# Optimization experiments

Hardware: AMD Instinct MI355X
Metric: run time of the kernel (lower is better)

## Reference

```python
import jax, jax.numpy as jnp
import numpy as np

GAMMA = 0.5
POLY_COEF = 0.1
POLY_DEGREE = 3


def setup_inputs() -> dict:
    key = jax.random.key(0)
    kx, ky = jax.random.split(key)
    x = jax.random.normal(kx, (8192, 256), dtype=jnp.float32)
    y = jax.random.normal(ky, (8192, 256), dtype=jnp.float32)
    return {"x": x, "y": y}


def reference(x, y):
    # K(x, y) = exp(-gamma * ||x - y||^2) + poly_coef * (x.y^T + 1)^degree
    xy = x @ y.T                                   # (N, M) GEMM
    x2 = jnp.sum(x * x, axis=-1, keepdims=True)    # (N, 1)
    y2 = jnp.sum(y * y, axis=-1)[None, :]          # (1, M)
    sqdist = jnp.maximum(x2 + y2 - 2.0 * xy, 0.0)
    rbf = jnp.exp(-GAMMA * sqdist)
    poly = POLY_COEF * (xy + 1.0) ** POLY_DEGREE
    return rbf + poly
```

## Files before the change

### kernel.cpp

```cpp
#include <hip/hip_runtime.h>
#include <hip/hip_bf16.h>
#include <cstdint>
#include <cstddef>


#define NROWS 8192
#define DK    256
#define BM    128
#define BN    128
#define BK    64

typedef __bf16 bf16_8 __attribute__((ext_vector_type(8)));
typedef float  f32x4  __attribute__((ext_vector_type(4)));

__device__ __forceinline__ unsigned short f2bf(float f) {
    unsigned int u = __builtin_bit_cast(unsigned int, f);
    u = (u + 0x7FFFu + ((u >> 16) & 1u)) >> 16;
    return (unsigned short)u;
}

__global__ __launch_bounds__(64) void prep_kernel(
    const float* __restrict__ x, const float* __restrict__ y,
    unsigned short* __restrict__ xb, unsigned short* __restrict__ yb,
    float* __restrict__ x2, float* __restrict__ y2)
{
    const int row  = blockIdx.x;
    const int lane = threadIdx.x;
    const size_t base = (size_t)row * DK + lane * 4;

    const float4 vx = *(const float4*)(x + base);
    const float4 vy = *(const float4*)(y + base);

    ushort4 hx = make_ushort4(f2bf(vx.x), f2bf(vx.y), f2bf(vx.z), f2bf(vx.w));
    ushort4 hy = make_ushort4(f2bf(vy.x), f2bf(vy.y), f2bf(vy.z), f2bf(vy.w));
    *(ushort4*)(xb + base) = hx;
    *(ushort4*)(yb + base) = hy;

    float sx = vx.x * vx.x + vx.y * vx.y + vx.z * vx.z + vx.w * vx.w;
    float sy = vy.x * vy.x + vy.y * vy.y + vy.z * vy.z + vy.w * vy.w;
    #pragma unroll
    for (int off = 32; off > 0; off >>= 1) {
        sx += __shfl_down(sx, off);
        sy += __shfl_down(sy, off);
    }
    if (lane == 0) {
        x2[row] = sx;
        y2[row] = sy;
    }
}

__global__ __launch_bounds__(256) void gemm_ep_kernel(
    const unsigned short* __restrict__ xb, const unsigned short* __restrict__ yb,
    const float* __restrict__ x2, const float* __restrict__ y2,
    float* __restrict__ out)
{
    __shared__ __align__(16) unsigned short As[BM * BK];
    __shared__ __align__(16) unsigned short Bs[BN * BK];

    const int tid  = threadIdx.x;
    const int wave = tid >> 6;
    const int lane = tid & 63;
    const int bm   = blockIdx.x;
    const int bn   = blockIdx.y;

    const int wm = (wave & 1) * 64;
    const int wn = (wave >> 1) * 64;

    const int subrow = lane >> 3;
    const int sslot  = (lane & 7) ^ subrow;
    const size_t laneoff = (size_t)subrow * DK + sslot * 8;

    const unsigned short* gA[4];
    const unsigned short* gB[4];
    unsigned short* lA[4];
    unsigned short* lB[4];
    #pragma unroll
    for (int m = 0; m < 4; ++m) {
        const int c = wave * 4 + m;
        gA[m] = xb + (size_t)(bm * BM + c * 8) * DK + laneoff;
        gB[m] = yb + (size_t)(bn * BN + c * 8) * DK + laneoff;
        lA[m] = &As[c * 512];
        lB[m] = &Bs[c * 512];
    }

    f32x4 acc[4][4];
    #pragma unroll
    for (int i = 0; i < 4; ++i)
        #pragma unroll
        for (int j = 0; j < 4; ++j)
            acc[i][j] = (f32x4){0.f, 0.f, 0.f, 0.f};

    const int quad = lane >> 4;
    const int l15  = lane & 15;
    const int l7   = l15 & 7;

    const int rbaseA = (wm + l15) * BK;
    const int rbaseB = (wn + l15) * BK;

    #pragma unroll
    for (int kt = 0; kt < DK; kt += BK) {
        #pragma unroll
        for (int m = 0; m < 4; ++m) {
            __builtin_amdgcn_global_load_lds(
                (const __attribute__((address_space(1))) void*)(gA[m] + kt),
                (__attribute__((address_space(3))) void*)lA[m], 16, 0, 0);
            __builtin_amdgcn_global_load_lds(
                (const __attribute__((address_space(1))) void*)(gB[m] + kt),
                (__attribute__((address_space(3))) void*)lB[m], 16, 0, 0);
        }
        __syncthreads();

        #pragma unroll
        for (int kk = 0; kk < 2; ++kk) {
            const int slot = ((kk << 2) | quad) ^ l7;
            bf16_8 afr[4], bfr[4];
            #pragma unroll
            for (int i = 0; i < 4; ++i)
                afr[i] = *(const bf16_8*)&As[rbaseA + i * 16 * BK + slot * 8];
            #pragma unroll
            for (int j = 0; j < 4; ++j)
                bfr[j] = *(const bf16_8*)&Bs[rbaseB + j * 16 * BK + slot * 8];

            #pragma unroll
            for (int i = 0; i < 4; ++i)
                #pragma unroll
                for (int j = 0; j < 4; ++j)
                    acc[i][j] = __builtin_amdgcn_mfma_f32_16x16x32_bf16(
                        afr[i], bfr[j], acc[i][j], 0, 0, 0);
        }
        __syncthreads();
    }

    const int mBase = bm * BM + wm + quad * 4;
    const int nBase = bn * BN + wn + l15;

    float y2v[4];
    #pragma unroll
    for (int j = 0; j < 4; ++j) y2v[j] = y2[nBase + j * 16];

    #pragma unroll
    for (int i = 0; i < 4; ++i) {
        #pragma unroll
        for (int r = 0; r < 4; ++r) {
            const int m = mBase + i * 16 + r;
            const float xv = x2[m];
            float* orow = out + (size_t)m * NROWS + nBase;
            #pragma unroll
            for (int j = 0; j < 4; ++j) {
                const float xy = acc[i][j][r];
                float s = xv + y2v[j] - 2.0f * xy;
                s = fmaxf(s, 0.0f);
                const float e = __expf(-0.5f * s);
                const float p = xy + 1.0f;
                orow[j * 16] = fmaf(0.1f, p * p * p, e);
            }
        }
    }
}

extern "C" void kernel_launch(void* const* d_in, const int* in_sizes, int n_in,
                              void* d_out, int out_size, void* d_ws, size_t ws_size,
                              hipStream_t stream) {
    const float* x = (const float*)d_in[0];
    const float* y = (const float*)d_in[1];
    float* out = (float*)d_out;

    char* ws = (char*)d_ws;
    unsigned short* xb = (unsigned short*)ws;
    unsigned short* yb = (unsigned short*)(ws + (size_t)NROWS * DK * 2);
    float* x2 = (float*)(ws + (size_t)2 * NROWS * DK * 2);
    float* y2 = x2 + NROWS;

    prep_kernel<<<NROWS, 64, 0, stream>>>(x, y, xb, yb, x2, y2);

    dim3 grid(NROWS / BM, NROWS / BN);
    gemm_ep_kernel<<<grid, 256, 0, stream>>>(xb, yb, x2, y2, out);
}
```

Baseline: 290.3 us.

## Load MFMA fragments directly from global memory and remap tiles per XCD

Drops the LDS staging and barriers. Each wave now loads its bf16 A/B MFMA fragments straight from global memory, relying on L2 and MALL caching for reuse across waves. Block IDs are remapped so that each XCD handles a contiguous 2D region of output tiles, which improves L2 locality. A launch-bounds occupancy hint of 2 is added. The trade-off is more redundant global or cache traffic per block in exchange for no shared-memory round trips or syncs; the output-write-bound epilogue is unchanged.

```diff
diff --git a/kernel.cpp b/kernel.cpp
--- a/kernel.cpp
+++ b/kernel.cpp
@@ -8,7 +8,6 @@
 #define DK    256
 #define BM    128
 #define BN    128
-#define BK    64
 
 typedef __bf16 bf16_8 __attribute__((ext_vector_type(8)));
 typedef float  f32x4  __attribute__((ext_vector_type(4)));
@@ -49,38 +48,33 @@
     }
 }
 
-__global__ __launch_bounds__(256) void gemm_ep_kernel(
+__global__ __launch_bounds__(256, 2) void gemm_ep_kernel(
     const unsigned short* __restrict__ xb, const unsigned short* __restrict__ yb,
     const float* __restrict__ x2, const float* __restrict__ y2,
     float* __restrict__ out)
 {
-    __shared__ __align__(16) unsigned short As[BM * BK];
-    __shared__ __align__(16) unsigned short Bs[BN * BK];
-
     const int tid  = threadIdx.x;
     const int wave = tid >> 6;
     const int lane = tid & 63;
-    const int bm   = blockIdx.x;
-    const int bn   = blockIdx.y;
+
+    const int id  = blockIdx.x;
+    const int xcd = id & 7;
+    const int idx = id >> 3;
+    const int bm  = (xcd & 1) * 32 + (idx & 31);
+    const int bn  = (xcd >> 1) * 16 + (idx >> 5);
 
     const int wm = (wave & 1) * 64;
     const int wn = (wave >> 1) * 64;
 
-    const int subrow = lane >> 3;
-    const int sslot  = (lane & 7) ^ subrow;
-    const size_t laneoff = (size_t)subrow * DK + sslot * 8;
+    const int quad = lane >> 4;
+    const int l15  = lane & 15;
 
     const unsigned short* gA[4];
     const unsigned short* gB[4];
-    unsigned short* lA[4];
-    unsigned short* lB[4];
     #pragma unroll
-    for (int m = 0; m < 4; ++m) {
-        const int c = wave * 4 + m;
-        gA[m] = xb + (size_t)(bm * BM + c * 8) * DK + laneoff;
-        gB[m] = yb + (size_t)(bn * BN + c * 8) * DK + laneoff;
-        lA[m] = &As[c * 512];
-        lB[m] = &Bs[c * 512];
+    for (int i = 0; i < 4; ++i) {
+        gA[i] = xb + (size_t)(bm * BM + wm + i * 16 + l15) * DK + quad * 8;
+        gB[i] = yb + (size_t)(bn * BN + wn + i * 16 + l15) * DK + quad * 8;
     }
 
     f32x4 acc[4][4];
@@ -90,45 +84,22 @@
         for (int j = 0; j < 4; ++j)
             acc[i][j] = (f32x4){0.f, 0.f, 0.f, 0.f};
 
-    const int quad = lane >> 4;
-    const int l15  = lane & 15;
-    const int l7   = l15 & 7;
-
-    const int rbaseA = (wm + l15) * BK;
-    const int rbaseB = (wn + l15) * BK;
-
     #pragma unroll
-    for (int kt = 0; kt < DK; kt += BK) {
+    for (int kt = 0; kt < DK; kt += 32) {
+        bf16_8 afr[4], bfr[4];
         #pragma unroll
-        for (int m = 0; m < 4; ++m) {
-            __builtin_amdgcn_global_load_lds(
-                (const __attribute__((address_space(1))) void*)(gA[m] + kt),
-                (__attribute__((address_space(3))) void*)lA[m], 16, 0, 0);
-            __builtin_amdgcn_global_load_lds(
-                (const __attribute__((address_space(1))) void*)(gB[m] + kt),
-                (__attribute__((address_space(3))) void*)lB[m], 16, 0, 0);
-        }
-        __syncthreads();
+        for (int i = 0; i < 4; ++i)
+            afr[i] = *(const bf16_8*)(gA[i] + kt);
+        #pragma unroll
+        for (int j = 0; j < 4; ++j)
+            bfr[j] = *(const bf16_8*)(gB[j] + kt);
 
         #pragma unroll
-        for (int kk = 0; kk < 2; ++kk) {
-            const int slot = ((kk << 2) | quad) ^ l7;
-            bf16_8 afr[4], bfr[4];
-            #pragma unroll
-            for (int i = 0; i < 4; ++i)
-                afr[i] = *(const bf16_8*)&As[rbaseA + i * 16 * BK + slot * 8];
+        for (int i = 0; i < 4; ++i)
             #pragma unroll
             for (int j = 0; j < 4; ++j)
-                bfr[j] = *(const bf16_8*)&Bs[rbaseB + j * 16 * BK + slot * 8];
-
-            #pragma unroll
-            for (int i = 0; i < 4; ++i)
-                #pragma unroll
-                for (int j = 0; j < 4; ++j)
-                    acc[i][j] = __builtin_amdgcn_mfma_f32_16x16x32_bf16(
-                        afr[i], bfr[j], acc[i][j], 0, 0, 0);
-        }
-        __syncthreads();
+                acc[i][j] = __builtin_amdgcn_mfma_f32_16x16x32_bf16(
+                    afr[i], bfr[j], acc[i][j], 0, 0, 0);
     }
 
     const int mBase = bm * BM + wm + quad * 4;
@@ -173,6 +144,5 @@
 
     prep_kernel<<<NROWS, 64, 0, stream>>>(x, y, xb, yb, x2, y2);
 
-    dim3 grid(NROWS / BM, NROWS / BN);
-    gemm_ep_kernel<<<grid, 256, 0, stream>>>(xb, yb, x2, y2, out);
+    gemm_ep_kernel<<<NROWS / BM * (NROWS / BN), 256, 0, stream>>>(xb, yb, x2, y2, out);
 }
```

Measured after the change: 367.2 us. 1.26x slower.
